# Kernel tuning notes

Measured on AMD Instinct MI355X. Metric: run time of the kernel, lower is better.

## Reference

```python
import jax, jax.numpy as jnp
import numpy as np

N, E, F, H, D, C = 50000, 800000, 128, 8, 16, 40


def setup_inputs() -> dict:
    key = jax.random.key(0)
    ks = jax.random.split(key, 12)
    s_in = 1.0 / np.sqrt(F)
    s_h = 1.0 / np.sqrt(H * D)
    return {
        "x": jax.random.normal(ks[0], (N, F), jnp.float32),
        "edge_index": jax.random.randint(ks[1], (2, E), 0, N, jnp.int64),
        "W1": jax.random.normal(ks[2], (F, H * D), jnp.float32) * s_in,
        "a_src1": jax.random.normal(ks[3], (H, D), jnp.float32) * s_h,
        "a_dst1": jax.random.normal(ks[4], (H, D), jnp.float32) * s_h,
        "b1": jnp.zeros((H * D,), jnp.float32),
        "W2": jax.random.normal(ks[5], (H * D, H * D), jnp.float32) * s_h,
        "a_src2": jax.random.normal(ks[6], (H, D), jnp.float32) * s_h,
        "a_dst2": jax.random.normal(ks[7], (H, D), jnp.float32) * s_h,
        "b2": jnp.zeros((H * D,), jnp.float32),
        "Wc": jax.random.normal(ks[8], (H * D, C), jnp.float32) * s_h,
        "bc": jnp.zeros((C,), jnp.float32),
    }


def _gat_layer(x, src, dst, W, a_src, a_dst, b):
    # x: [N, F_in]; src/dst: [E'] (self-loops already appended)
    n = x.shape[0]
    h, d = a_src.shape
    hx = (x @ W).reshape(n, h, d)                      # [N, H, D]
    al_src = jnp.einsum("nhd,hd->nh", hx, a_src)       # [N, H]
    al_dst = jnp.einsum("nhd,hd->nh", hx, a_dst)       # [N, H]
    e = jax.nn.leaky_relu(al_src[src] + al_dst[dst], 0.2)  # [E', H]
    # segment softmax over incoming edges of each destination node
    m = jax.ops.segment_max(e, dst, num_segments=n)    # [N, H]
    e = jnp.exp(e - m[dst])
    z = jax.ops.segment_sum(e, dst, num_segments=n)    # [N, H]
    alpha = e / z[dst]                                 # [E', H]
    out = jax.ops.segment_sum(alpha[:, :, None] * hx[src], dst, num_segments=n)
    return out.reshape(n, h * d) + b


def reference(x, edge_index, W1, a_src1, a_dst1, b1, W2, a_src2, a_dst2, b2, Wc, bc):
    n = x.shape[0]
    loops = jnp.arange(n, dtype=edge_index.dtype)
    src = jnp.concatenate([edge_index[0], loops])  # PyG GATConv adds self-loops
    dst = jnp.concatenate([edge_index[1], loops])
    h = _gat_layer(x, src, dst, W1, a_src1, a_dst1, b1)
    h = jax.nn.elu(h)  # ELU between layers (i < K-1); dropout=None -> no-op
    h = _gat_layer(h, src, dst, W2, a_src2, a_dst2, b2)
    return h @ Wc + bc  # [N, C] logits
```

## Files before the change

### kernel.cpp

```cpp
#include <hip/hip_runtime.h>
#include <hip/hip_bf16.h>
#include <hip/hip_fp16.h>


#define FDIM 128
#define HEADS 8

typedef short bf16x8 __attribute__((ext_vector_type(8)));
typedef float f32x4 __attribute__((ext_vector_type(4)));

__device__ __forceinline__ float leaky02(float x) {
    return fmaxf(x, 0.2f * x);
}

__device__ __forceinline__ unsigned pack2h(float x, float y) {
    __half2 h2 = __floats2half2_rn(x, y);
    return *(unsigned*)&h2;
}

__device__ __forceinline__ void split2(float x, unsigned short& hi, unsigned short& lo) {
    unsigned bits = __float_as_uint(x);
    unsigned h = bits + 0x7fffu + ((bits >> 16) & 1u);
    hi = (unsigned short)(h >> 16);
    float hf = __uint_as_float(h & 0xffff0000u);
    float r = x - hf;
    unsigned rb = __float_as_uint(r);
    unsigned l2 = rb + 0x7fffu + ((rb >> 16) & 1u);
    lo = (unsigned short)(l2 >> 16);
}


__global__ __launch_bounds__(256) void wconv_kernel(const float* __restrict__ W1,
                                                    const float* __restrict__ W2,
                                                    unsigned short* __restrict__ w1_hi,
                                                    unsigned short* __restrict__ w1_lo,
                                                    unsigned short* __restrict__ w2_hi,
                                                    unsigned short* __restrict__ w2_lo) {
    int b = blockIdx.x, t = threadIdx.x;
    const float* W = (b < 16) ? W1 : W2;
    unsigned short* whi = (b < 16) ? w1_hi : w2_hi;
    unsigned short* wlo = (b < 16) ? w1_lo : w2_lo;
    int idx = (b & 15) * 256 + t;
    int k = idx >> 5;
    int c0 = (idx & 31) * 4;
#pragma unroll
    for (int i = 0; i < 4; ++i) {
        int c = c0 + i;
        float v = W[k * FDIM + c];
        unsigned short h, l;
        split2(v, h, l);
        int dest = ((k >> 5) * 8 + (c >> 4)) * 512 +
                   ((c & 15) + (((k >> 3) & 3) << 4)) * 8 + (k & 7);
        whi[dest] = h;
        wlo[dest] = l;
    }
}


__global__ __launch_bounds__(256) void scan_partial(const int* __restrict__ deg,
                                                    int* __restrict__ partials,
                                                    int n) {
    __shared__ int red[256];
    int t = threadIdx.x;
    int base = blockIdx.x * 1024 + t * 4;
    int s = 0;
#pragma unroll
    for (int j = 0; j < 4; ++j) {
        int i = base + j;
        if (i < n) s += deg[i];
    }
    red[t] = s;
    __syncthreads();
    for (int off = 128; off > 0; off >>= 1) {
        if (t < off) red[t] += red[t + off];
        __syncthreads();
    }
    if (t == 0) partials[blockIdx.x] = red[0];
}

__global__ __launch_bounds__(256) void scan_final(const int* __restrict__ deg,
                                                  const int* __restrict__ partials,
                                                  int* __restrict__ row_start,
                                                  int n, int nb) {
    __shared__ int sbuf[256];
    __shared__ int boff_s, total_s;
    int t = threadIdx.x;
    if (t < 64) {
        int carry = 0;
        for (int base = 0; base < nb; base += 64) {
            int idx = base + t;
            int v = (idx < nb) ? partials[idx] : 0;
            int incl = v;
#pragma unroll
            for (int off = 1; off < 64; off <<= 1) {
                int x = __shfl_up(incl, off);
                if (t >= off) incl += x;
            }
            if (idx == (int)blockIdx.x) boff_s = carry + incl - v;
            carry += __shfl(incl, 63);
        }
        if (t == 0) total_s = carry;
    }
    __syncthreads();
    if (blockIdx.x == 0 && t == 0) row_start[n] = total_s;

    int base = blockIdx.x * 1024 + t * 4;
    int v[4];
#pragma unroll
    for (int j = 0; j < 4; ++j) v[j] = (base + j < n) ? deg[base + j] : 0;
    int tsum = v[0] + v[1] + v[2] + v[3];
    sbuf[t] = tsum;
    __syncthreads();
    for (int off = 1; off < 256; off <<= 1) {
        int tmp = (t >= off) ? sbuf[t - off] : 0;
        __syncthreads();
        sbuf[t] += tmp;
        __syncthreads();
    }
    int toff = boff_s + sbuf[t] - tsum;
    int run = 0;
#pragma unroll
    for (int j = 0; j < 4; ++j) {
        int i = base + j;
        if (i < n) row_start[i] = toff + run;
        run += v[j];
    }
}


__global__ __launch_bounds__(256) void scatter_kernel(const int* __restrict__ ei,
                                                      const int* __restrict__ rank,
                                                      const int* __restrict__ row_start,
                                                      int* __restrict__ csr_src,
                                                      int E) {
    int tid = threadIdx.x;
#pragma unroll
    for (int j = 0; j < 4; ++j) {
        int e = blockIdx.x * 1024 + j * 256 + tid;
        if (e < E) {
            int s = ei[e];
            int d = ei[E + e];
            __builtin_nontemporal_store(s, &csr_src[row_start[d] + rank[e]]);
        }
    }
}


template <bool FUSED>
__global__ __launch_bounds__(256, 4) void gemm_mfma(const float* __restrict__ xf,
                                                    const unsigned short* __restrict__ a_hi,
                                                    const unsigned short* __restrict__ a_lo,
                                                    const unsigned short* __restrict__ w_hi,
                                                    const unsigned short* __restrict__ w_lo,
                                                    const float* __restrict__ asrc,
                                                    const float* __restrict__ adst,
                                                    float* __restrict__ als,
                                                    float* __restrict__ ald,
                                                    unsigned* __restrict__ hxf,
                                                    int n,
                                                    const int* __restrict__ ei,
                                                    int* __restrict__ deg,
                                                    int* __restrict__ rank,
                                                    int E, int ng, int grid) {
    int tid = threadIdx.x;
    int gb;
    if (FUSED) {
        int bid = blockIdx.x;
        int t0 = (int)((long long)bid * ng / grid);
        int t1 = (int)((long long)(bid + 1) * ng / grid);
        if (t1 == t0) {
            int sb = bid - t0;
#pragma unroll
            for (int j = 0; j < 4; ++j) {
                int e = sb * 1024 + j * 256 + tid;
                if (e < E) rank[e] = atomicAdd(&deg[ei[E + e]], 1);
            }
            return;
        }
        gb = t0;
    } else {
        gb = blockIdx.x;
    }

    int lane = tid & 63;
    int wave = tid >> 6;
    int l15 = lane & 15;
    int lg = lane >> 4;
    int row0 = gb * 32;

    f32x4 acc[2][2];
#pragma unroll
    for (int fr = 0; fr < 2; ++fr)
#pragma unroll
        for (int fc = 0; fc < 2; ++fc)
#pragma unroll
            for (int r = 0; r < 4; ++r) acc[fr][fc][r] = 0.f;

#pragma unroll
    for (int kc = 0; kc < 4; ++kc) {
        bf16x8 Ah[2], Al[2], Bh[2], Bl[2];
#pragma unroll
        for (int fr = 0; fr < 2; ++fr) {
            int r = row0 + fr * 16 + l15;
            if (r > n - 1) r = n - 1;
            if (FUSED) {
                const float* px = xf + (size_t)r * FDIM + kc * 32 + lg * 8;
                float4 v0 = *(const float4*)px;
                float4 v1 = *(const float4*)(px + 4);
                float vv[8] = {v0.x, v0.y, v0.z, v0.w, v1.x, v1.y, v1.z, v1.w};
#pragma unroll
                for (int j = 0; j < 8; ++j) {
                    unsigned bits = __float_as_uint(vv[j]);
                    Ah[fr][j] = (short)(bits >> 16);
                    float hf = __uint_as_float(bits & 0xffff0000u);
                    Al[fr][j] = (short)(__float_as_uint(vv[j] - hf) >> 16);
                }
            } else {
                size_t off = (size_t)r * FDIM + kc * 32 + lg * 8;
                Ah[fr] = *(const bf16x8*)(a_hi + off);
                Al[fr] = *(const bf16x8*)(a_lo + off);
            }
        }
#pragma unroll
        for (int fc = 0; fc < 2; ++fc) {
            int FC = wave * 2 + fc;
            size_t off = (size_t)(kc * 8 + FC) * 512 + lane * 8;
            Bh[fc] = *(const bf16x8*)(w_hi + off);
            Bl[fc] = *(const bf16x8*)(w_lo + off);
        }
#pragma unroll
        for (int fr = 0; fr < 2; ++fr)
#pragma unroll
            for (int fc = 0; fc < 2; ++fc) {
                acc[fr][fc] = __builtin_amdgcn_mfma_f32_16x16x32_bf16(
                    Al[fr], Bh[fc], acc[fr][fc], 0, 0, 0);
                acc[fr][fc] = __builtin_amdgcn_mfma_f32_16x16x32_bf16(
                    Ah[fr], Bl[fc], acc[fr][fc], 0, 0, 0);
                acc[fr][fc] = __builtin_amdgcn_mfma_f32_16x16x32_bf16(
                    Ah[fr], Bh[fc], acc[fr][fc], 0, 0, 0);
            }
    }

#pragma unroll
    for (int fr = 0; fr < 2; ++fr)
#pragma unroll
        for (int fc = 0; fc < 2; ++fc) {
            int CB = wave * 32 + fc * 16;
            int col = CB + l15;
            float as_ = asrc[col];
            float ad_ = adst[col];
#pragma unroll
            for (int reg = 0; reg < 4; ++reg) {
                int row = row0 + fr * 16 + lg * 4 + reg;
                float v = acc[fr][fc][reg];
                float vn = __shfl_xor(v, 1);
                if ((lane & 1) == 0 && row < n)
                    hxf[(size_t)row * 64 + (col >> 1)] = pack2h(v, vn);
                float ps = v * as_;
                float pd = v * ad_;
                ps += __shfl_xor(ps, 1);
                pd += __shfl_xor(pd, 1);
                ps += __shfl_xor(ps, 2);
                pd += __shfl_xor(pd, 2);
                ps += __shfl_xor(ps, 4);
                pd += __shfl_xor(pd, 4);
                ps += __shfl_xor(ps, 8);
                pd += __shfl_xor(pd, 8);
                if (l15 == 0 && row < n) {
                    als[row * HEADS + (CB >> 4)] = ps;
                    ald[row * HEADS + (CB >> 4)] = pd;
                }
            }
        }
}


__global__ __launch_bounds__(256, 8) void gemm_cls(const unsigned* __restrict__ h_f16,
                                                   const float* __restrict__ W,
                                                   const float* __restrict__ bias,
                                                   float* __restrict__ out,
                                                   int n) {
    __shared__ float xs[32][136];
    __shared__ float ws[32][48];
    int tid = threadIdx.x;
    int row0 = blockIdx.x * 128;
    int lane = tid & 63;
    int wave = tid >> 6;
    int lane2 = lane * 2;
    int wc = wave * 10;

    float acc[2][10];
#pragma unroll
    for (int i = 0; i < 2; ++i)
#pragma unroll
        for (int j = 0; j < 10; ++j) acc[i][j] = 0.f;

    for (int kc = 0; kc < 128; kc += 32) {
        if (kc) __syncthreads();
#pragma unroll
        for (int it = 0; it < 4; ++it) {
            int idx = it * 256 + tid;
            int r = idx >> 3, kg = (idx & 7) * 4;
            float4 v = make_float4(0.f, 0.f, 0.f, 0.f);
            if (row0 + r < n) {
                uint2 hh = *(const uint2*)&h_f16[(size_t)(row0 + r) * 64 + (kc + kg) / 2];
                float2 a = __half22float2(*(__half2*)&hh.x);
                float2 b = __half22float2(*(__half2*)&hh.y);
                v.x = a.x; v.y = a.y; v.z = b.x; v.w = b.y;
            }
            int col = r ^ kg;
            xs[kg + 0][col] = v.x;
            xs[kg + 1][col] = v.y;
            xs[kg + 2][col] = v.z;
            xs[kg + 3][col] = v.w;
        }
#pragma unroll
        for (int it = 0; it < 6; ++it) {
            int idx = it * 256 + tid;
            int kk = idx / 48, c = idx - kk * 48;
            ws[kk][c] = (c < 40) ? W[(size_t)(kc + kk) * 40 + c] : 0.f;
        }
        __syncthreads();
#pragma unroll
        for (int k = 0; k < 32; ++k) {
            int s = ((k >> 2) & 7) << 2;
            float2 av2 = *(const float2*)&xs[k][lane2 ^ s];
            float av[2] = {av2.x, av2.y};
#pragma unroll
            for (int j = 0; j < 10; ++j) {
                float w = ws[k][wc + j];
                acc[0][j] += av[0] * w;
                acc[1][j] += av[1] * w;
            }
        }
    }

#pragma unroll
    for (int i = 0; i < 2; ++i) {
        int row = row0 + lane2 + i;
        if (row < n) {
#pragma unroll
            for (int j = 0; j < 10; ++j)
                out[(size_t)row * 40 + wc + j] = acc[i][j] + bias[wc + j];
        }
    }
}


template <bool DOELU, bool WRITELO>
__global__ __launch_bounds__(256) void gat_aggregate(const unsigned* __restrict__ hxf,
                                                     const float* __restrict__ als,
                                                     const float* __restrict__ ald,
                                                     const int* __restrict__ row_start,
                                                     const int* __restrict__ csr_src,
                                                     const float* __restrict__ bias,
                                                     unsigned* __restrict__ h_hi,
                                                     unsigned* __restrict__ h_lo,
                                                     int n) {
    int wid = threadIdx.x >> 6;
    int lane = threadIdx.x & 63;
    int node = blockIdx.x * 4 + wid;
    if (node >= n) return;

    int rs = row_start[node];
    int deg = row_start[node + 1] - rs;

    int h = lane & 7;
    int hc = lane >> 3;
    int lq = lane >> 3;
    float ald_h = ald[node * HEADS + h];

    float acc0 = 0.f, acc1 = 0.f, zown = 0.f;
    int total = deg + 1;

    int ii = lq;
    int srcv = (ii < deg) ? csr_src[rs + ii] : node;
    float w = (ii < total) ? __expf(leaky02(als[srcv * HEADS + h] + ald_h)) : 0.f;

    int i0 = 0;
    for (; i0 + 8 <= total; i0 += 8) {
        zown += w;
        int ii_n = i0 + 8 + lq;
        int srcv_n = (ii_n < deg) ? csr_src[rs + ii_n] : node;
#pragma unroll
        for (int e = 0; e < 8; ++e) {
            int s = __builtin_amdgcn_readlane(srcv, e * 8);
            float we = __shfl(w, e * 8 + hc);
            unsigned v = hxf[(size_t)s * 64 + lane];
            float2 f = __half22float2(*(__half2*)&v);
            acc0 += we * f.x;
            acc1 += we * f.y;
        }
        float w_n = (ii_n < total) ? __expf(leaky02(als[srcv_n * HEADS + h] + ald_h)) : 0.f;
        srcv = srcv_n;
        w = w_n;
    }
    int rem = total - i0;
    if (rem > 0) {
        zown += w;
        for (int e = 0; e < rem; ++e) {
            int s = __builtin_amdgcn_readlane(srcv, e * 8);
            float we = __shfl(w, e * 8 + hc);
            unsigned v = hxf[(size_t)s * 64 + lane];
            float2 f = __half22float2(*(__half2*)&v);
            acc0 += we * f.x;
            acc1 += we * f.y;
        }
    }

    zown += __shfl_xor(zown, 8);
    zown += __shfl_xor(zown, 16);
    zown += __shfl_xor(zown, 32);
    float z = __shfl(zown, hc);

    float2 bv = *(const float2*)&bias[2 * lane];
    float o0 = acc0 / z + bv.x;
    float o1 = acc1 / z + bv.y;
    if (DOELU) {
        o0 = o0 > 0.f ? o0 : (__expf(o0) - 1.f);
        o1 = o1 > 0.f ? o1 : (__expf(o1) - 1.f);
    }
    if (WRITELO) {
        unsigned short hh0, ll0, hh1, ll1;
        split2(o0, hh0, ll0);
        split2(o1, hh1, ll1);
        h_hi[(size_t)node * 64 + lane] = (unsigned)hh0 | ((unsigned)hh1 << 16);
        h_lo[(size_t)node * 64 + lane] = (unsigned)ll0 | ((unsigned)ll1 << 16);
    } else {
        h_hi[(size_t)node * 64 + lane] = pack2h(o0, o1);
    }
}


extern "C" void kernel_launch(void* const* d_in, const int* in_sizes, int n_in,
                              void* d_out, int out_size, void* d_ws, size_t ws_size,
                              hipStream_t stream) {
    const float* x      = (const float*)d_in[0];
    const int*   ei     = (const int*)d_in[1];
    const float* W1     = (const float*)d_in[2];
    const float* a_src1 = (const float*)d_in[3];
    const float* a_dst1 = (const float*)d_in[4];
    const float* b1     = (const float*)d_in[5];
    const float* W2     = (const float*)d_in[6];
    const float* a_src2 = (const float*)d_in[7];
    const float* a_dst2 = (const float*)d_in[8];
    const float* b2     = (const float*)d_in[9];
    const float* Wc     = (const float*)d_in[10];
    const float* bc     = (const float*)d_in[11];
    float* out = (float*)d_out;

    const int N = in_sizes[0] / FDIM;
    const int E = in_sizes[1] / 2;
    const int NB = (N + 1023) / 1024;
    const int nel = N * FDIM;
    (void)nel;

    unsigned* hxf = (unsigned*)d_ws;
    unsigned* xh_u = hxf + (size_t)N * 64;
    unsigned* xl_u = xh_u + (size_t)N * 64;
    float* als  = (float*)(xl_u + (size_t)N * 64);
    float* ald  = als + (size_t)N * HEADS;
    unsigned short* w1_hi = (unsigned short*)(ald + (size_t)N * HEADS);
    unsigned short* w1_lo = w1_hi + 16384;
    unsigned short* w2_hi = w1_lo + 16384;
    unsigned short* w2_lo = w2_hi + 16384;
    int* deg       = (int*)(w2_lo + 16384);
    int* row_start = deg + N;
    int* partials  = row_start + ((N + 8) & ~3);
    int* rank      = partials + ((NB + 4) & ~3);
    int* csr_src   = rank + E;

    hipMemsetAsync(deg, 0, (size_t)N * sizeof(int), stream);
    wconv_kernel<<<32, 256, 0, stream>>>(W1, W2, w1_hi, w1_lo, w2_hi, w2_lo);

    const int ng = (N + 31) / 32;
    const int hb = (E + 1023) / 1024;
    const int grid1 = ng + hb;
    const int agg_grid = (N + 3) / 4;
    const int cls_grid = (N + 127) / 128;

    gemm_mfma<true><<<grid1, 256, 0, stream>>>(x, nullptr, nullptr,
                                               w1_hi, w1_lo,
                                               a_src1, a_dst1, als, ald, hxf, N,
                                               ei, deg, rank, E, ng, grid1);
    scan_partial<<<NB, 256, 0, stream>>>(deg, partials, N);
    scan_final<<<NB, 256, 0, stream>>>(deg, partials, row_start, N, NB);
    scatter_kernel<<<hb, 256, 0, stream>>>(ei, rank, row_start, csr_src, E);

    gat_aggregate<true, true><<<agg_grid, 256, 0, stream>>>(
        hxf, als, ald, row_start, csr_src, b1, xh_u, xl_u, N);
    gemm_mfma<false><<<ng, 256, 0, stream>>>(nullptr,
                                             (const unsigned short*)xh_u,
                                             (const unsigned short*)xl_u,
                                             w2_hi, w2_lo,
                                             a_src2, a_dst2, als, ald, hxf, N,
                                             nullptr, nullptr, nullptr, 0, ng, ng);
    gat_aggregate<false, false><<<agg_grid, 256, 0, stream>>>(
        hxf, als, ald, row_start, csr_src, b2, xh_u, xl_u, N);
    gemm_cls<<<cls_grid, 256, 0, stream>>>(xh_u, Wc, bc, out, N);
}
```

Baseline: 222.9 us.

## Stage GEMM operand tiles through LDS with async global-to-LDS loads

The MFMA GEMM now copies its A-tile (bf16 hi/lo halves, or raw fp32 in the fused path) into shared memory with global_load_lds before the k-loop. It also double-buffers the weight hi/lo fragments in LDS, prefetching the next k-chunk while computing the current one. Registers are then filled from LDS rather than from direct global vector loads, aiming to overlap memory latency with MFMA work. In exchange it uses 48 KB of LDS per block, adds a barrier every k-step, and relaxes launch bounds from 4 to 3 blocks per SM, which lowers occupancy for a GEMM that is a small share of the total pipeline.

```diff
diff --git a/kernel.cpp b/kernel.cpp
--- a/kernel.cpp
+++ b/kernel.cpp
@@ -8,6 +8,13 @@
 
 typedef short bf16x8 __attribute__((ext_vector_type(8)));
 typedef float f32x4 __attribute__((ext_vector_type(4)));
+
+typedef __attribute__((address_space(1))) const unsigned gu32;
+typedef __attribute__((address_space(3))) unsigned lu32;
+
+__device__ __forceinline__ void load_lds16(const void* g, void* l) {
+    __builtin_amdgcn_global_load_lds((gu32*)g, (lu32*)l, 16, 0, 0);
+}
 
 __device__ __forceinline__ float leaky02(float x) {
     return fmaxf(x, 0.2f * x);
@@ -147,7 +154,7 @@
 
 
 template <bool FUSED>
-__global__ __launch_bounds__(256, 4) void gemm_mfma(const float* __restrict__ xf,
+__global__ __launch_bounds__(256, 3) void gemm_mfma(const float* __restrict__ xf,
                                                     const unsigned short* __restrict__ a_hi,
                                                     const unsigned short* __restrict__ a_lo,
                                                     const unsigned short* __restrict__ w_hi,
@@ -162,6 +169,7 @@
                                                     int* __restrict__ deg,
                                                     int* __restrict__ rank,
                                                     int E, int ng, int grid) {
+    __shared__ __align__(16) char smem[49152];
     int tid = threadIdx.x;
     int gb;
     if (FUSED) {
@@ -188,6 +196,37 @@
     int lg = lane >> 4;
     int row0 = gb * 32;
 
+    {
+#pragma unroll
+        for (int c = 0; c < 4; ++c) {
+            int s = wave * 4 + c;
+            int kc = s >> 2, fr = (s >> 1) & 1, p = s & 1;
+            int rg = row0 + fr * 16 + l15;
+            if (rg > n - 1) rg = n - 1;
+            if (FUSED) {
+                load_lds16(xf + (size_t)rg * FDIM + kc * 32 + lg * 8 + p * 4,
+                           smem + (size_t)s * 1024);
+            } else {
+                const unsigned short* src = p ? a_lo : a_hi;
+                load_lds16(src + (size_t)rg * FDIM + kc * 32 + lg * 8,
+                           smem + (size_t)s * 1024);
+            }
+        }
+    }
+
+    auto stage_B = [&](int kc, int buf) {
+#pragma unroll
+        for (int c = 0; c < 4; ++c) {
+            int s = wave * 4 + c;
+            int FC = s >> 1, p = s & 1;
+            const unsigned short* src = p ? w_lo : w_hi;
+            load_lds16(src + (size_t)(kc * 8 + FC) * 512 + lane * 8,
+                       smem + 16384 + (size_t)buf * 16384 + (size_t)(FC * 2 + p) * 1024);
+        }
+    };
+    stage_B(0, 0);
+    __syncthreads();
+
     f32x4 acc[2][2];
 #pragma unroll
     for (int fr = 0; fr < 2; ++fr)
@@ -198,15 +237,15 @@
 
 #pragma unroll
     for (int kc = 0; kc < 4; ++kc) {
-        bf16x8 Ah[2], Al[2], Bh[2], Bl[2];
+        const int cur = kc & 1;
+        if (kc < 3) stage_B(kc + 1, cur ^ 1);
+
+        bf16x8 Ah[2], Al[2];
 #pragma unroll
         for (int fr = 0; fr < 2; ++fr) {
-            int r = row0 + fr * 16 + l15;
-            if (r > n - 1) r = n - 1;
             if (FUSED) {
-                const float* px = xf + (size_t)r * FDIM + kc * 32 + lg * 8;
-                float4 v0 = *(const float4*)px;
-                float4 v1 = *(const float4*)(px + 4);
+                const float4 v0 = *(const float4*)(smem + (size_t)(kc * 4 + fr * 2) * 1024 + lane * 16);
+                const float4 v1 = *(const float4*)(smem + (size_t)(kc * 4 + fr * 2 + 1) * 1024 + lane * 16);
                 float vv[8] = {v0.x, v0.y, v0.z, v0.w, v1.x, v1.y, v1.z, v1.w};
 #pragma unroll
                 for (int j = 0; j < 8; ++j) {
@@ -216,17 +255,17 @@
                     Al[fr][j] = (short)(__float_as_uint(vv[j] - hf) >> 16);
                 }
             } else {
-                size_t off = (size_t)r * FDIM + kc * 32 + lg * 8;
-                Ah[fr] = *(const bf16x8*)(a_hi + off);
-                Al[fr] = *(const bf16x8*)(a_lo + off);
-            }
-        }
+                Ah[fr] = *(const bf16x8*)(smem + (size_t)(kc * 4 + fr * 2) * 1024 + lane * 16);
+                Al[fr] = *(const bf16x8*)(smem + (size_t)(kc * 4 + fr * 2 + 1) * 1024 + lane * 16);
+            }
+        }
+        bf16x8 Bh[2], Bl[2];
 #pragma unroll
         for (int fc = 0; fc < 2; ++fc) {
             int FC = wave * 2 + fc;
-            size_t off = (size_t)(kc * 8 + FC) * 512 + lane * 8;
-            Bh[fc] = *(const bf16x8*)(w_hi + off);
-            Bl[fc] = *(const bf16x8*)(w_lo + off);
+            const char* bb = smem + 16384 + (size_t)cur * 16384 + (size_t)(FC * 2) * 1024;
+            Bh[fc] = *(const bf16x8*)(bb + lane * 16);
+            Bl[fc] = *(const bf16x8*)(bb + 1024 + lane * 16);
         }
 #pragma unroll
         for (int fr = 0; fr < 2; ++fr)
@@ -239,6 +278,7 @@
                 acc[fr][fc] = __builtin_amdgcn_mfma_f32_16x16x32_bf16(
                     Ah[fr], Bh[fc], acc[fr][fc], 0, 0, 0);
             }
+        __syncthreads();
     }
 
 #pragma unroll
@@ -452,8 +492,6 @@
     const int N = in_sizes[0] / FDIM;
     const int E = in_sizes[1] / 2;
     const int NB = (N + 1023) / 1024;
-    const int nel = N * FDIM;
-    (void)nel;
 
     unsigned* hxf = (unsigned*)d_ws;
     unsigned* xh_u = hxf + (size_t)N * 64;
```

Result: faster. 217.7 us (-2.3%).
